# Kernel optimization log

Measured on AMD Instinct MI355X. Metric: run time of the kernel, lower is better.

## Reference

```python
import jax, jax.numpy as jnp
import numpy as np

DIM = 1024
HEADS = 16
HEAD_DIM = DIM // HEADS


def setup_inputs() -> dict:
    key = jax.random.key(0)
    ks = jax.random.split(key, 5)
    s = 1.0 / np.sqrt(DIM)
    x = jax.random.normal(ks[0], (2, 2048, DIM), dtype=jnp.float32)
    # torch nn.Linear weights are [out_features, in_features]
    W_qkv = jax.random.uniform(ks[1], (3 * DIM, DIM), dtype=jnp.float32, minval=-s, maxval=s)
    b_qkv = jax.random.uniform(ks[2], (3 * DIM,), dtype=jnp.float32, minval=-s, maxval=s)
    W_out = jax.random.uniform(ks[3], (DIM, DIM), dtype=jnp.float32, minval=-s, maxval=s)
    b_out = jax.random.uniform(ks[4], (DIM,), dtype=jnp.float32, minval=-s, maxval=s)
    return {"x": x, "W_qkv": W_qkv, "b_qkv": b_qkv, "W_out": W_out, "b_out": b_out}


def reference(x, W_qkv, b_qkv, W_out, b_out):
    B, N, D = x.shape
    qkv = jnp.einsum('bnd,ed->bne', x, W_qkv) + b_qkv            # [B,N,3D]
    qkv = qkv.reshape(B, N, 3, HEADS, HEAD_DIM)
    qkv = jnp.transpose(qkv, (2, 0, 3, 1, 4))                    # [3,B,H,N,hd]
    q, k, v = qkv[0], qkv[1], qkv[2]
    scale = 1.0 / np.sqrt(HEAD_DIM).astype(np.float32)
    attn = jnp.einsum('bhnd,bhmd->bhnm', q, k) * scale           # [B,H,N,N]
    attn = jax.nn.softmax(attn, axis=-1)
    out = jnp.einsum('bhnm,bhmd->bhnd', attn, v)                 # [B,H,N,hd]
    out = jnp.transpose(out, (0, 2, 1, 3)).reshape(B, N, D)
    out = jnp.einsum('bnd,ed->bne', out, W_out) + b_out
    return out
```

## Files before the change

### kernel.cpp

```cpp
#include <hip/hip_runtime.h>
#include <stdint.h>
#include <stddef.h>

typedef __attribute__((ext_vector_type(4))) float  f32x4;
typedef __attribute__((ext_vector_type(8))) short  s16x8;
typedef __attribute__((ext_vector_type(4))) float  float4v;
typedef __attribute__((ext_vector_type(4))) unsigned short u16x4;
typedef __attribute__((ext_vector_type(2))) unsigned int   u32x2;

#define DIM    1024
#define HEADS  16
#define HD     64
#define SEQ    2048
#define BATCH  2
#define TOKENS (BATCH * SEQ)

#define QSCALE 0.18033688011112042f

__device__ __forceinline__ unsigned short f2bf(float f) {
  union { float f; uint32_t u; } x; x.f = f;
  uint32_t r = x.u + 0x7fffu + ((x.u >> 16) & 1u);
  return (unsigned short)(r >> 16);
}

__device__ __forceinline__ float fast_exp2(float x) {
#if __has_builtin(__builtin_amdgcn_exp2f)
  return __builtin_amdgcn_exp2f(x);
#else
  return exp2f(x);
#endif
}

__device__ __forceinline__ uint32_t pack_bf16_trunc(uint32_t lo, uint32_t hi) {
#if __has_builtin(__builtin_amdgcn_perm)
  return __builtin_amdgcn_perm(hi, lo, 0x07060302u);
#else
  return (hi & 0xffff0000u) | (lo >> 16);
#endif
}

__device__ __forceinline__ void stage16(const unsigned short* gp, unsigned short* lp) {
#if __has_builtin(__builtin_amdgcn_global_load_lds)
  __builtin_amdgcn_global_load_lds((const __attribute__((address_space(1))) void*)gp,
                                   (__attribute__((address_space(3))) void*)lp, 16, 0, 0);
#else
  *(s16x8*)(lp + (threadIdx.x & 63) * 8) = *(const s16x8*)gp;
#endif
}

#define N4_X  (TOKENS * DIM / 4)
#define N4_WQ (3 * DIM * DIM / 4)
#define N4_WO (DIM * DIM / 4)
__global__ __launch_bounds__(256) void mhsa_cast_all(const float* __restrict__ x,
    const float* __restrict__ wq, const float* __restrict__ wo,
    unsigned short* __restrict__ xb, unsigned short* __restrict__ wqb,
    unsigned short* __restrict__ wob) {
  int i = blockIdx.x * 256 + threadIdx.x;
  const float* src; unsigned short* dst; int off;
  if (i < N4_X)              { src = x;  dst = xb;  off = i; }
  else if (i < N4_X + N4_WQ) { src = wq; dst = wqb; off = i - N4_X; }
  else                       { src = wo; dst = wob; off = i - (N4_X + N4_WQ); }
  float4v f = ((const float4v*)src)[off];
  u16x4 o;
  o.x = f2bf(f.x); o.y = f2bf(f.y); o.z = f2bf(f.z); o.w = f2bf(f.w);
  ((u16x4*)dst)[off] = o;
}

__global__ __launch_bounds__(256) void mhsa_gemm_qkv(const unsigned short* __restrict__ A,
    const unsigned short* __restrict__ Bw, const float* __restrict__ bias,
    unsigned short* __restrict__ qws, unsigned short* __restrict__ kws,
    unsigned short* __restrict__ vws) {
  __shared__ unsigned short As[128 * 32];
  __shared__ unsigned short Bs[128 * 32];
  const int t = threadIdx.x;
  const int w = t >> 6, l = t & 63;
  const int wm = w >> 1, wn = w & 1;
  const int rowBase = blockIdx.y * 128;
  const int colBase = blockIdx.x * 128;
  const int fr = l & 15, fc = (l >> 4) * 8;
  const int crow = l >> 2, ccol = (l & 3) * 8;

  f32x4 zero = {0.f, 0.f, 0.f, 0.f};
  f32x4 acc[4][4];
  #pragma unroll
  for (int a = 0; a < 4; ++a)
    #pragma unroll
    for (int b = 0; b < 4; ++b) acc[a][b] = zero;

  for (int k0 = 0; k0 < DIM; k0 += 32) {
    __syncthreads();
    #pragma unroll
    for (int it = 0; it < 2; ++it) {
      const int c = w * 2 + it;
      stage16(A  + (size_t)(rowBase + c * 16 + crow) * DIM + k0 + ccol, &As[c * 512]);
      stage16(Bw + (size_t)(colBase + c * 16 + crow) * DIM + k0 + ccol, &Bs[c * 512]);
    }
    __syncthreads();
    s16x8 xf[4], wf[4];
    #pragma unroll
    for (int b = 0; b < 4; ++b) xf[b] = *(const s16x8*)&As[(wm * 64 + b * 16 + fr) * 32 + fc];
    #pragma unroll
    for (int a = 0; a < 4; ++a) wf[a] = *(const s16x8*)&Bs[(wn * 64 + a * 16 + fr) * 32 + fc];
    #pragma unroll
    for (int a = 0; a < 4; ++a)
      #pragma unroll
      for (int b = 0; b < 4; ++b)
        acc[a][b] = __builtin_amdgcn_mfma_f32_16x16x32_bf16(wf[a], xf[b], acc[a][b], 0, 0, 0);
  }

  const int q4 = l >> 4, ln = l & 15;
  const int which = colBase >> 10;
  const float sc = (which == 0) ? QSCALE : 1.0f;
  unsigned short* dst = (which == 0) ? qws : ((which == 1) ? kws : vws);

  #pragma unroll
  for (int a = 0; a < 4; ++a) {
    const int e0 = colBase + wn * 64 + a * 16 + q4 * 4;
    const float4v bs4 = *(const float4v*)&bias[e0];
    const int rr0 = e0 & 1023;
    const int h = rr0 >> 6, d0 = rr0 & 63;
    #pragma unroll
    for (int b = 0; b < 4; ++b) {
      const int tok = rowBase + wm * 64 + b * 16 + ln;
      const int bb = tok >> 11, n = tok & 2047;
      if (which != 2) {
        u16x4 pk;
        #pragma unroll
        for (int r = 0; r < 4; ++r) pk[r] = f2bf((acc[a][b][r] + bs4[r]) * sc);
        *(u16x4*)&dst[(((size_t)(bb * HEADS + h)) * SEQ + n) * HD + d0] = pk;
      } else {
        #pragma unroll
        for (int r = 0; r < 4; ++r)
          dst[(((size_t)(bb * HEADS + h)) * HD + d0 + r) * SEQ + n] =
              f2bf(acc[a][b][r] + bs4[r]);
      }
    }
  }
}

__global__ __launch_bounds__(256) void mhsa_gemm_out(const unsigned short* __restrict__ A,
    const unsigned short* __restrict__ Bw, const float* __restrict__ bias,
    float* __restrict__ out) {
  __shared__ unsigned short As[128 * 32];
  __shared__ unsigned short Bs[128 * 32];
  const int t = threadIdx.x;
  const int w = t >> 6, l = t & 63;
  const int wm = w >> 1, wn = w & 1;
  const int rowBase = blockIdx.y * 128;
  const int colBase = blockIdx.x * 128;
  const int fr = l & 15, fc = (l >> 4) * 8;
  const int crow = l >> 2, ccol = (l & 3) * 8;

  f32x4 zero = {0.f, 0.f, 0.f, 0.f};
  f32x4 acc[4][4];
  #pragma unroll
  for (int a = 0; a < 4; ++a)
    #pragma unroll
    for (int b = 0; b < 4; ++b) acc[a][b] = zero;

  for (int k0 = 0; k0 < DIM; k0 += 32) {
    __syncthreads();
    #pragma unroll
    for (int it = 0; it < 2; ++it) {
      const int c = w * 2 + it;
      stage16(A  + (size_t)(rowBase + c * 16 + crow) * DIM + k0 + ccol, &As[c * 512]);
      stage16(Bw + (size_t)(colBase + c * 16 + crow) * DIM + k0 + ccol, &Bs[c * 512]);
    }
    __syncthreads();
    s16x8 xf[4], wf[4];
    #pragma unroll
    for (int b = 0; b < 4; ++b) xf[b] = *(const s16x8*)&As[(wm * 64 + b * 16 + fr) * 32 + fc];
    #pragma unroll
    for (int a = 0; a < 4; ++a) wf[a] = *(const s16x8*)&Bs[(wn * 64 + a * 16 + fr) * 32 + fc];
    #pragma unroll
    for (int a = 0; a < 4; ++a)
      #pragma unroll
      for (int b = 0; b < 4; ++b)
        acc[a][b] = __builtin_amdgcn_mfma_f32_16x16x32_bf16(wf[a], xf[b], acc[a][b], 0, 0, 0);
  }

  const int q4 = l >> 4, ln = l & 15;
  #pragma unroll
  for (int a = 0; a < 4; ++a) {
    const int e0 = colBase + wn * 64 + a * 16 + q4 * 4;
    const float4v bs4 = *(const float4v*)&bias[e0];
    #pragma unroll
    for (int b = 0; b < 4; ++b) {
      const int tok = rowBase + wm * 64 + b * 16 + ln;
      float4v v;
      #pragma unroll
      for (int r = 0; r < 4; ++r) v[r] = acc[a][b][r] + bs4[r];
      *(float4v*)&out[(size_t)tok * DIM + e0] = v;
    }
  }
}

__global__ __launch_bounds__(256, 2) void mhsa_attn(const unsigned short* __restrict__ q,
    const unsigned short* __restrict__ k, const unsigned short* __restrict__ vt,
    unsigned short* __restrict__ o) {
  __shared__ unsigned short QPs[4 * 32 * 72];
  __shared__ unsigned short Ks[2][64 * 64];
  __shared__ unsigned short Vs[2][64 * 64];
  const int t = threadIdx.x, w = t >> 6, l = t & 63;
  const int q4 = l >> 4, ln = l & 15;
  const int bh = blockIdx.y, q0 = blockIdx.x * 128;
  const unsigned short* qb  = q  + (size_t)bh * SEQ * HD;
  const unsigned short* kb  = k  + (size_t)bh * SEQ * HD;
  const unsigned short* vtb = vt + (size_t)bh * HD * SEQ;

  const int srow = l >> 3;
  const int scol = ((l & 7) ^ srow) * 8;

  unsigned short* Pw = &QPs[w * (32 * 72)];

  #pragma unroll
  for (int it = 0; it < 4; ++it)
    stage16(qb + (size_t)(q0 + w * 32 + it * 8 + srow) * HD + scol, &Pw[it * 512]);
  #pragma unroll
  for (int it = 0; it < 2; ++it) {
    const int c = w + it * 4;
    stage16(kb  + (size_t)(c * 8 + srow) * HD + scol, &Ks[0][c * 512]);
    stage16(vtb + (size_t)(c * 8 + srow) * SEQ + scol, &Vs[0][c * 512]);
  }
  __syncthreads();

  s16x8 aq[2][2];
  #pragma unroll
  for (int i = 0; i < 2; ++i)
    #pragma unroll
    for (int kk = 0; kk < 2; ++kk)
      aq[i][kk] = *(const s16x8*)&Pw[(i * 16 + ln) * 64 + (((kk * 4 + q4) ^ (ln & 7)) * 8)];

  f32x4 zero = {0.f, 0.f, 0.f, 0.f};
  f32x4 accO[2][4];
  float lsum[2] = {0.f, 0.f};
  #pragma unroll
  for (int i = 0; i < 2; ++i)
    #pragma unroll
    for (int jd = 0; jd < 4; ++jd) accO[i][jd] = zero;

  for (int jt = 0; jt < SEQ / 64; ++jt) {
    const int cur = jt & 1, nxt = cur ^ 1;
    if (jt + 1 < SEQ / 64) {
      const int j1 = (jt + 1) * 64;
      #pragma unroll
      for (int it = 0; it < 2; ++it) {
        const int c = w + it * 4;
        stage16(kb  + (size_t)(j1 + c * 8 + srow) * HD + scol, &Ks[nxt][c * 512]);
        stage16(vtb + (size_t)(c * 8 + srow) * SEQ + j1 + scol, &Vs[nxt][c * 512]);
      }
    }

    f32x4 St[4][2];
    #pragma unroll
    for (int jb = 0; jb < 4; ++jb)
      #pragma unroll
      for (int i = 0; i < 2; ++i) St[jb][i] = zero;
    #pragma unroll
    for (int jb = 0; jb < 4; ++jb) {
      s16x8 ak0 = *(const s16x8*)&Ks[cur][(jb * 16 + ln) * 64 + ((q4 ^ (ln & 7)) * 8)];
      s16x8 ak1 = *(const s16x8*)&Ks[cur][(jb * 16 + ln) * 64 + (((4 + q4) ^ (ln & 7)) * 8)];
      #pragma unroll
      for (int i = 0; i < 2; ++i) {
        St[jb][i] = __builtin_amdgcn_mfma_f32_16x16x32_bf16(ak0, aq[i][0], St[jb][i], 0, 0, 0);
        St[jb][i] = __builtin_amdgcn_mfma_f32_16x16x32_bf16(ak1, aq[i][1], St[jb][i], 0, 0, 0);
      }
    }

    #pragma unroll
    for (int i = 0; i < 2; ++i)
      #pragma unroll
      for (int jb = 0; jb < 4; ++jb) {
        uint32_t u0 = __float_as_uint(fast_exp2(St[jb][i][0]));
        uint32_t u1 = __float_as_uint(fast_exp2(St[jb][i][1]));
        uint32_t u2 = __float_as_uint(fast_exp2(St[jb][i][2]));
        uint32_t u3 = __float_as_uint(fast_exp2(St[jb][i][3]));
        lsum[i] += __uint_as_float(u0 & 0xffff0000u) + __uint_as_float(u1 & 0xffff0000u)
                 + __uint_as_float(u2 & 0xffff0000u) + __uint_as_float(u3 & 0xffff0000u);
        u32x2 pk;
        pk.x = pack_bf16_trunc(u0, u1);
        pk.y = pack_bf16_trunc(u2, u3);
        *(u32x2*)&Pw[(i * 16 + ln) * 72 + jb * 16 + q4 * 4] = pk;
      }

    s16x8 ap[2][2];
    #pragma unroll
    for (int i = 0; i < 2; ++i)
      #pragma unroll
      for (int kk = 0; kk < 2; ++kk)
        ap[i][kk] = *(const s16x8*)&Pw[(i * 16 + ln) * 72 + kk * 32 + q4 * 8];

    #pragma unroll
    for (int jd = 0; jd < 4; ++jd) {
      s16x8 bv0 = *(const s16x8*)&Vs[cur][(jd * 16 + ln) * 64 + ((q4 ^ (ln & 7)) * 8)];
      s16x8 bv1 = *(const s16x8*)&Vs[cur][(jd * 16 + ln) * 64 + (((4 + q4) ^ (ln & 7)) * 8)];
      #pragma unroll
      for (int i = 0; i < 2; ++i) {
        accO[i][jd] = __builtin_amdgcn_mfma_f32_16x16x32_bf16(ap[i][0], bv0, accO[i][jd], 0, 0, 0);
        accO[i][jd] = __builtin_amdgcn_mfma_f32_16x16x32_bf16(ap[i][1], bv1, accO[i][jd], 0, 0, 0);
      }
    }

    __syncthreads();
  }

  const int b = bh >> 4, h = bh & 15;
  #pragma unroll
  for (int i = 0; i < 2; ++i) {
    float s = lsum[i];
    s += __shfl_xor(s, 16);
    s += __shfl_xor(s, 32);
    const float inv = 1.f / s;
    #pragma unroll
    for (int r = 0; r < 4; ++r) {
      const float invr = __shfl(inv, (l & 48) + q4 * 4 + r);
      const int row = q0 + w * 32 + i * 16 + q4 * 4 + r;
      #pragma unroll
      for (int jd = 0; jd < 4; ++jd)
        o[((size_t)(b * SEQ + row)) * DIM + h * HD + jd * 16 + ln] = f2bf(accO[i][jd][r] * invr);
    }
  }
}

extern "C" void kernel_launch(void* const* d_in, const int* in_sizes, int n_in,
                              void* d_out, int out_size, void* d_ws, size_t ws_size,
                              hipStream_t stream) {
  const float* x     = (const float*)d_in[0];
  const float* Wqkv  = (const float*)d_in[1];
  const float* bqkv  = (const float*)d_in[2];
  const float* Wout  = (const float*)d_in[3];
  const float* bout  = (const float*)d_in[4];
  float* out = (float*)d_out;

  unsigned short* ws = (unsigned short*)d_ws;
  unsigned short* x_bf    = ws;
  unsigned short* wqkv_bf = x_bf    + (size_t)TOKENS * DIM;
  unsigned short* wout_bf = wqkv_bf + (size_t)3 * DIM * DIM;
  unsigned short* q_ws    = wout_bf + (size_t)DIM * DIM;
  unsigned short* k_ws    = q_ws    + (size_t)TOKENS * DIM;
  unsigned short* v_ws    = k_ws    + (size_t)TOKENS * DIM;
  unsigned short* ao_ws   = v_ws    + (size_t)TOKENS * DIM;

  {
    const int n4 = N4_X + N4_WQ + N4_WO;
    mhsa_cast_all<<<n4 / 256, 256, 0, stream>>>(x, Wqkv, Wout, x_bf, wqkv_bf, wout_bf);
  }

  {
    dim3 grid(3 * DIM / 128, TOKENS / 128);
    mhsa_gemm_qkv<<<grid, 256, 0, stream>>>(x_bf, wqkv_bf, bqkv, q_ws, k_ws, v_ws);
  }

  {
    dim3 grid(SEQ / 128, BATCH * HEADS);
    mhsa_attn<<<grid, 256, 0, stream>>>(q_ws, k_ws, v_ws, ao_ws);
  }

  {
    dim3 grid(DIM / 128, TOKENS / 128);
    mhsa_gemm_out<<<grid, 256, 0, stream>>>(ao_ws, wout_bf, bout, out);
  }
}
```

Baseline: 212.1 us.

## Double-buffer GEMM LDS tiles with BK=64 and XOR-swizzled layout

Both projection GEMMs now stage 64-wide K tiles into two LDS buffers, so the load of the next tile is issued while MFMAs run on the current one. This halves the number of K iterations and drops one barrier per iteration. An XOR swizzle on the 16-byte column chunks is meant to avoid LDS bank conflicts on the fragment reads. The cost is 4x the LDS per block (64 KB), which may limit how many blocks fit on a CU.

Result: no change. 210.2 us (-0.9%).

```diff
diff --git a/kernel.cpp b/kernel.cpp
--- a/kernel.cpp
+++ b/kernel.cpp
@@ -66,19 +66,21 @@
   ((u16x4*)dst)[off] = o;
 }
 
+
 __global__ __launch_bounds__(256) void mhsa_gemm_qkv(const unsigned short* __restrict__ A,
     const unsigned short* __restrict__ Bw, const float* __restrict__ bias,
     unsigned short* __restrict__ qws, unsigned short* __restrict__ kws,
     unsigned short* __restrict__ vws) {
-  __shared__ unsigned short As[128 * 32];
-  __shared__ unsigned short Bs[128 * 32];
+  __shared__ unsigned short As[2][128 * 64];
+  __shared__ unsigned short Bs[2][128 * 64];
   const int t = threadIdx.x;
   const int w = t >> 6, l = t & 63;
   const int wm = w >> 1, wn = w & 1;
   const int rowBase = blockIdx.y * 128;
   const int colBase = blockIdx.x * 128;
-  const int fr = l & 15, fc = (l >> 4) * 8;
-  const int crow = l >> 2, ccol = (l & 3) * 8;
+  const int fr = l & 15, q4 = l >> 4, ln = l & 15;
+  const int srow = l >> 3;
+  const int scol = ((l & 7) ^ srow) * 8;
 
   f32x4 zero = {0.f, 0.f, 0.f, 0.f};
   f32x4 acc[4][4];
@@ -87,28 +89,43 @@
     #pragma unroll
     for (int b = 0; b < 4; ++b) acc[a][b] = zero;
 
-  for (int k0 = 0; k0 < DIM; k0 += 32) {
+  #pragma unroll
+  for (int it = 0; it < 4; ++it) {
+    const int c = w * 4 + it;
+    stage16(A  + (size_t)(rowBase + c * 8 + srow) * DIM + scol, &As[0][c * 512]);
+    stage16(Bw + (size_t)(colBase + c * 8 + srow) * DIM + scol, &Bs[0][c * 512]);
+  }
+  __syncthreads();
+
+  for (int kt = 0; kt < DIM / 64; ++kt) {
+    const int cur = kt & 1, nxt = cur ^ 1;
+    if (kt + 1 < DIM / 64) {
+      const int k1 = (kt + 1) * 64;
+      #pragma unroll
+      for (int it = 0; it < 4; ++it) {
+        const int c = w * 4 + it;
+        stage16(A  + (size_t)(rowBase + c * 8 + srow) * DIM + k1 + scol, &As[nxt][c * 512]);
+        stage16(Bw + (size_t)(colBase + c * 8 + srow) * DIM + k1 + scol, &Bs[nxt][c * 512]);
+      }
+    }
+    #pragma unroll
+    for (int kk = 0; kk < 2; ++kk) {
+      s16x8 xf[4], wf[4];
+      #pragma unroll
+      for (int b = 0; b < 4; ++b)
+        xf[b] = *(const s16x8*)&As[cur][(wm * 64 + b * 16 + fr) * 64 + (((kk * 4 + q4) ^ (fr & 7)) * 8)];
+      #pragma unroll
+      for (int a = 0; a < 4; ++a)
+        wf[a] = *(const s16x8*)&Bs[cur][(wn * 64 + a * 16 + fr) * 64 + (((kk * 4 + q4) ^ (fr & 7)) * 8)];
+      #pragma unroll
+      for (int a = 0; a < 4; ++a)
+        #pragma unroll
+        for (int b = 0; b < 4; ++b)
+          acc[a][b] = __builtin_amdgcn_mfma_f32_16x16x32_bf16(wf[a], xf[b], acc[a][b], 0, 0, 0);
+    }
     __syncthreads();
-    #pragma unroll
-    for (int it = 0; it < 2; ++it) {
-      const int c = w * 2 + it;
-      stage16(A  + (size_t)(rowBase + c * 16 + crow) * DIM + k0 + ccol, &As[c * 512]);
-      stage16(Bw + (size_t)(colBase + c * 16 + crow) * DIM + k0 + ccol, &Bs[c * 512]);
-    }
-    __syncthreads();
-    s16x8 xf[4], wf[4];
-    #pragma unroll
-    for (int b = 0; b < 4; ++b) xf[b] = *(const s16x8*)&As[(wm * 64 + b * 16 + fr) * 32 + fc];
-    #pragma unroll
-    for (int a = 0; a < 4; ++a) wf[a] = *(const s16x8*)&Bs[(wn * 64 + a * 16 + fr) * 32 + fc];
-    #pragma unroll
-    for (int a = 0; a < 4; ++a)
-      #pragma unroll
-      for (int b = 0; b < 4; ++b)
-        acc[a][b] = __builtin_amdgcn_mfma_f32_16x16x32_bf16(wf[a], xf[b], acc[a][b], 0, 0, 0);
-  }
-
-  const int q4 = l >> 4, ln = l & 15;
+  }
+
   const int which = colBase >> 10;
   const float sc = (which == 0) ? QSCALE : 1.0f;
   unsigned short* dst = (which == 0) ? qws : ((which == 1) ? kws : vws);
@@ -141,15 +158,16 @@
 __global__ __launch_bounds__(256) void mhsa_gemm_out(const unsigned short* __restrict__ A,
     const unsigned short* __restrict__ Bw, const float* __restrict__ bias,
     float* __restrict__ out) {
-  __shared__ unsigned short As[128 * 32];
-  __shared__ unsigned short Bs[128 * 32];
+  __shared__ unsigned short As[2][128 * 64];
+  __shared__ unsigned short Bs[2][128 * 64];
   const int t = threadIdx.x;
   const int w = t >> 6, l = t & 63;
   const int wm = w >> 1, wn = w & 1;
   const int rowBase = blockIdx.y * 128;
   const int colBase = blockIdx.x * 128;
-  const int fr = l & 15, fc = (l >> 4) * 8;
-  const int crow = l >> 2, ccol = (l & 3) * 8;
+  const int fr = l & 15, q4 = l >> 4, ln = l & 15;
+  const int srow = l >> 3;
+  const int scol = ((l & 7) ^ srow) * 8;
 
   f32x4 zero = {0.f, 0.f, 0.f, 0.f};
   f32x4 acc[4][4];
@@ -158,28 +176,43 @@
     #pragma unroll
     for (int b = 0; b < 4; ++b) acc[a][b] = zero;
 
-  for (int k0 = 0; k0 < DIM; k0 += 32) {
+  #pragma unroll
+  for (int it = 0; it < 4; ++it) {
+    const int c = w * 4 + it;
+    stage16(A  + (size_t)(rowBase + c * 8 + srow) * DIM + scol, &As[0][c * 512]);
+    stage16(Bw + (size_t)(colBase + c * 8 + srow) * DIM + scol, &Bs[0][c * 512]);
+  }
+  __syncthreads();
+
+  for (int kt = 0; kt < DIM / 64; ++kt) {
+    const int cur = kt & 1, nxt = cur ^ 1;
+    if (kt + 1 < DIM / 64) {
+      const int k1 = (kt + 1) * 64;
+      #pragma unroll
+      for (int it = 0; it < 4; ++it) {
+        const int c = w * 4 + it;
+        stage16(A  + (size_t)(rowBase + c * 8 + srow) * DIM + k1 + scol, &As[nxt][c * 512]);
+        stage16(Bw + (size_t)(colBase + c * 8 + srow) * DIM + k1 + scol, &Bs[nxt][c * 512]);
+      }
+    }
+    #pragma unroll
+    for (int kk = 0; kk < 2; ++kk) {
+      s16x8 xf[4], wf[4];
+      #pragma unroll
+      for (int b = 0; b < 4; ++b)
+        xf[b] = *(const s16x8*)&As[cur][(wm * 64 + b * 16 + fr) * 64 + (((kk * 4 + q4) ^ (fr & 7)) * 8)];
+      #pragma unroll
+      for (int a = 0; a < 4; ++a)
+        wf[a] = *(const s16x8*)&Bs[cur][(wn * 64 + a * 16 + fr) * 64 + (((kk * 4 + q4) ^ (fr & 7)) * 8)];
+      #pragma unroll
+      for (int a = 0; a < 4; ++a)
+        #pragma unroll
+        for (int b = 0; b < 4; ++b)
+          acc[a][b] = __builtin_amdgcn_mfma_f32_16x16x32_bf16(wf[a], xf[b], acc[a][b], 0, 0, 0);
+    }
     __syncthreads();
-    #pragma unroll
-    for (int it = 0; it < 2; ++it) {
-      const int c = w * 2 + it;
-      stage16(A  + (size_t)(rowBase + c * 16 + crow) * DIM + k0 + ccol, &As[c * 512]);
-      stage16(Bw + (size_t)(colBase + c * 16 + crow) * DIM + k0 + ccol, &Bs[c * 512]);
-    }
-    __syncthreads();
-    s16x8 xf[4], wf[4];
-    #pragma unroll
-    for (int b = 0; b < 4; ++b) xf[b] = *(const s16x8*)&As[(wm * 64 + b * 16 + fr) * 32 + fc];
-    #pragma unroll
-    for (int a = 0; a < 4; ++a) wf[a] = *(const s16x8*)&Bs[(wn * 64 + a * 16 + fr) * 32 + fc];
-    #pragma unroll
-    for (int a = 0; a < 4; ++a)
-      #pragma unroll
-      for (int b = 0; b < 4; ++b)
-        acc[a][b] = __builtin_amdgcn_mfma_f32_16x16x32_bf16(wf[a], xf[b], acc[a][b], 0, 0, 0);
-  }
-
-  const int q4 = l >> 4, ln = l & 15;
+  }
+
   #pragma unroll
   for (int a = 0; a < 4; ++a) {
     const int e0 = colBase + wn * 64 + a * 16 + q4 * 4;
```

## Double-buffer LDS in projection GEMMs, swizzle tiles, shrink out-proj tile

Applied to the files above, without the earlier changes.

Both projection GEMMs now double-buffer their shared-memory tiles, so the next K slice is staged while MFMAs run on the current one. This removes one barrier per iteration. An XOR swizzle on the column chunk is meant to avoid LDS bank conflicts on fragment reads. The output projection uses 64-row tiles so it launches more blocks and fills more CUs. The cost is double the LDS per block, and the smaller tile gives less reuse per block in the output GEMM.

Result: faster. 200.6 us (-5.4%).

```diff
diff --git a/kernel.cpp b/kernel.cpp
--- a/kernel.cpp
+++ b/kernel.cpp
@@ -66,19 +66,21 @@
   ((u16x4*)dst)[off] = o;
 }
 
-__global__ __launch_bounds__(256) void mhsa_gemm_qkv(const unsigned short* __restrict__ A,
+
+__global__ __launch_bounds__(256, 3) void mhsa_gemm_qkv(const unsigned short* __restrict__ A,
     const unsigned short* __restrict__ Bw, const float* __restrict__ bias,
     unsigned short* __restrict__ qws, unsigned short* __restrict__ kws,
     unsigned short* __restrict__ vws) {
-  __shared__ unsigned short As[128 * 32];
-  __shared__ unsigned short Bs[128 * 32];
+  __shared__ unsigned short As[2][128 * 32];
+  __shared__ unsigned short Bs[2][128 * 32];
   const int t = threadIdx.x;
   const int w = t >> 6, l = t & 63;
   const int wm = w >> 1, wn = w & 1;
   const int rowBase = blockIdx.y * 128;
   const int colBase = blockIdx.x * 128;
-  const int fr = l & 15, fc = (l >> 4) * 8;
-  const int crow = l >> 2, ccol = (l & 3) * 8;
+  const int fr = l & 15, q4 = l >> 4, ln = l & 15;
+  const int srow = l >> 2;
+  const int scol = ((l & 3) ^ (srow & 3)) * 8;
 
   f32x4 zero = {0.f, 0.f, 0.f, 0.f};
   f32x4 acc[4][4];
@@ -87,28 +89,40 @@
     #pragma unroll
     for (int b = 0; b < 4; ++b) acc[a][b] = zero;
 
-  for (int k0 = 0; k0 < DIM; k0 += 32) {
-    __syncthreads();
-    #pragma unroll
-    for (int it = 0; it < 2; ++it) {
-      const int c = w * 2 + it;
-      stage16(A  + (size_t)(rowBase + c * 16 + crow) * DIM + k0 + ccol, &As[c * 512]);
-      stage16(Bw + (size_t)(colBase + c * 16 + crow) * DIM + k0 + ccol, &Bs[c * 512]);
-    }
-    __syncthreads();
+  #pragma unroll
+  for (int it = 0; it < 2; ++it) {
+    const int c = w * 2 + it;
+    stage16(A  + (size_t)(rowBase + c * 16 + srow) * DIM + scol, &As[0][c * 512]);
+    stage16(Bw + (size_t)(colBase + c * 16 + srow) * DIM + scol, &Bs[0][c * 512]);
+  }
+  __syncthreads();
+
+  for (int kt = 0; kt < DIM / 32; ++kt) {
+    const int cur = kt & 1, nxt = cur ^ 1;
+    if (kt + 1 < DIM / 32) {
+      const int k1 = (kt + 1) * 32;
+      #pragma unroll
+      for (int it = 0; it < 2; ++it) {
+        const int c = w * 2 + it;
+        stage16(A  + (size_t)(rowBase + c * 16 + srow) * DIM + k1 + scol, &As[nxt][c * 512]);
+        stage16(Bw + (size_t)(colBase + c * 16 + srow) * DIM + k1 + scol, &Bs[nxt][c * 512]);
+      }
+    }
     s16x8 xf[4], wf[4];
     #pragma unroll
-    for (int b = 0; b < 4; ++b) xf[b] = *(const s16x8*)&As[(wm * 64 + b * 16 + fr) * 32 + fc];
-    #pragma unroll
-    for (int a = 0; a < 4; ++a) wf[a] = *(const s16x8*)&Bs[(wn * 64 + a * 16 + fr) * 32 + fc];
+    for (int b = 0; b < 4; ++b)
+      xf[b] = *(const s16x8*)&As[cur][(wm * 64 + b * 16 + fr) * 32 + ((q4 ^ (fr & 3)) * 8)];
+    #pragma unroll
+    for (int a = 0; a < 4; ++a)
+      wf[a] = *(const s16x8*)&Bs[cur][(wn * 64 + a * 16 + fr) * 32 + ((q4 ^ (fr & 3)) * 8)];
     #pragma unroll
     for (int a = 0; a < 4; ++a)
       #pragma unroll
       for (int b = 0; b < 4; ++b)
         acc[a][b] = __builtin_amdgcn_mfma_f32_16x16x32_bf16(wf[a], xf[b], acc[a][b], 0, 0, 0);
-  }
-
-  const int q4 = l >> 4, ln = l & 15;
+    __syncthreads();
+  }
+
   const int which = colBase >> 10;
   const float sc = (which == 0) ? QSCALE : 1.0f;
   unsigned short* dst = (which == 0) ? qws : ((which == 1) ? kws : vws);
@@ -138,55 +152,68 @@
   }
 }
 
-__global__ __launch_bounds__(256) void mhsa_gemm_out(const unsigned short* __restrict__ A,
+__global__ __launch_bounds__(256, 3) void mhsa_gemm_out(const unsigned short* __restrict__ A,
     const unsigned short* __restrict__ Bw, const float* __restrict__ bias,
     float* __restrict__ out) {
-  __shared__ unsigned short As[128 * 32];
-  __shared__ unsigned short Bs[128 * 32];
+  __shared__ unsigned short As[2][64 * 32];
+  __shared__ unsigned short Bs[2][128 * 32];
   const int t = threadIdx.x;
   const int w = t >> 6, l = t & 63;
   const int wm = w >> 1, wn = w & 1;
-  const int rowBase = blockIdx.y * 128;
+  const int rowBase = blockIdx.y * 64;
   const int colBase = blockIdx.x * 128;
-  const int fr = l & 15, fc = (l >> 4) * 8;
-  const int crow = l >> 2, ccol = (l & 3) * 8;
+  const int fr = l & 15, q4 = l >> 4, ln = l & 15;
+  const int srow = l >> 2;
+  const int scol = ((l & 3) ^ (srow & 3)) * 8;
 
   f32x4 zero = {0.f, 0.f, 0.f, 0.f};
-  f32x4 acc[4][4];
+  f32x4 acc[4][2];
   #pragma unroll
   for (int a = 0; a < 4; ++a)
     #pragma unroll
-    for (int b = 0; b < 4; ++b) acc[a][b] = zero;
-
-  for (int k0 = 0; k0 < DIM; k0 += 32) {
+    for (int b = 0; b < 2; ++b) acc[a][b] = zero;
+
+  #pragma unroll
+  for (int it = 0; it < 3; ++it) {
+    const int s = w * 3 + it;
+    if (s < 4) stage16(A  + (size_t)(rowBase + s * 16 + srow) * DIM + scol, &As[0][s * 512]);
+    else       stage16(Bw + (size_t)(colBase + (s - 4) * 16 + srow) * DIM + scol, &Bs[0][(s - 4) * 512]);
+  }
+  __syncthreads();
+
+  for (int kt = 0; kt < DIM / 32; ++kt) {
+    const int cur = kt & 1, nxt = cur ^ 1;
+    if (kt + 1 < DIM / 32) {
+      const int k1 = (kt + 1) * 32;
+      #pragma unroll
+      for (int it = 0; it < 3; ++it) {
+        const int s = w * 3 + it;
+        if (s < 4) stage16(A  + (size_t)(rowBase + s * 16 + srow) * DIM + k1 + scol, &As[nxt][s * 512]);
+        else       stage16(Bw + (size_t)(colBase + (s - 4) * 16 + srow) * DIM + k1 + scol, &Bs[nxt][(s - 4) * 512]);
+      }
+    }
+    s16x8 xf[2], wf[4];
+    #pragma unroll
+    for (int b = 0; b < 2; ++b)
+      xf[b] = *(const s16x8*)&As[cur][(wm * 32 + b * 16 + fr) * 32 + ((q4 ^ (fr & 3)) * 8)];
+    #pragma unroll
+    for (int a = 0; a < 4; ++a)
+      wf[a] = *(const s16x8*)&Bs[cur][(wn * 64 + a * 16 + fr) * 32 + ((q4 ^ (fr & 3)) * 8)];
+    #pragma unroll
+    for (int a = 0; a < 4; ++a)
+      #pragma unroll
+      for (int b = 0; b < 2; ++b)
+        acc[a][b] = __builtin_amdgcn_mfma_f32_16x16x32_bf16(wf[a], xf[b], acc[a][b], 0, 0, 0);
     __syncthreads();
-    #pragma unroll
-    for (int it = 0; it < 2; ++it) {
-      const int c = w * 2 + it;
-      stage16(A  + (size_t)(rowBase + c * 16 + crow) * DIM + k0 + ccol, &As[c * 512]);
-      stage16(Bw + (size_t)(colBase + c * 16 + crow) * DIM + k0 + ccol, &Bs[c * 512]);
-    }
-    __syncthreads();
-    s16x8 xf[4], wf[4];
-    #pragma unroll
-    for (int b = 0; b < 4; ++b) xf[b] = *(const s16x8*)&As[(wm * 64 + b * 16 + fr) * 32 + fc];
-    #pragma unroll
-    for (int a = 0; a < 4; ++a) wf[a] = *(const s16x8*)&Bs[(wn * 64 + a * 16 + fr) * 32 + fc];
-    #pragma unroll
-    for (int a = 0; a < 4; ++a)
-      #pragma unroll
-      for (int b = 0; b < 4; ++b)
-        acc[a][b] = __builtin_amdgcn_mfma_f32_16x16x32_bf16(wf[a], xf[b], acc[a][b], 0, 0, 0);
-  }
-
-  const int q4 = l >> 4, ln = l & 15;
+  }
+
   #pragma unroll
   for (int a = 0; a < 4; ++a) {
     const int e0 = colBase + wn * 64 + a * 16 + q4 * 4;
     const float4v bs4 = *(const float4v*)&bias[e0];
     #pragma unroll
-    for (int b = 0; b < 4; ++b) {
-      const int tok = rowBase + wm * 64 + b * 16 + ln;
+    for (int b = 0; b < 2; ++b) {
+      const int tok = rowBase + wm * 32 + b * 16 + ln;
       float4v v;
       #pragma unroll
       for (int r = 0; r < 4; ++r) v[r] = acc[a][b][r] + bs4[r];
@@ -357,7 +384,7 @@
   }
 
   {
-    dim3 grid(DIM / 128, TOKENS / 128);
+    dim3 grid(DIM / 128, TOKENS / 64);
     mhsa_gemm_out<<<grid, 256, 0, stream>>>(ao_ws, wout_bf, bout, out);
   }
 }
```
